# Kernel tuning notes

Hardware: AMD Instinct MI355X
Metric: run time of the kernel (lower is better)

The kernel has to match this reference:

```python
import jax, jax.numpy as jnp
import numpy as np

B, N, C = 2, 2048, 1024
H = 16
R = 4
MLP = 4096
LORA_SCALE = 1.0 / R  # lora_alpha=1, r=4
EPS = 1e-5


def _ln(x, g, b):
    m = jnp.mean(x, axis=-1, keepdims=True)
    v = jnp.mean(jnp.square(x - m), axis=-1, keepdims=True)
    return (x - m) * jax.lax.rsqrt(v + EPS) * g + b


def setup_inputs() -> dict:
    key = jax.random.key(0)
    ks = jax.random.split(key, 16)
    s = lambda k, shape, fan: jax.random.normal(k, shape, jnp.float32) * (1.0 / np.sqrt(fan))
    return {
        "x": jax.random.normal(ks[0], (B, N, C), jnp.float32),
        "pos": jax.random.normal(ks[1], (B, N, C), jnp.float32),
        "Wqkv": s(ks[2], (3 * C, C), C),
        "b_qkv": jnp.zeros((3 * C,), jnp.float32),
        "lora_A": s(ks[3], (2 * R, C), C),          # rows 0:R -> q, R:2R -> v
        "lora_B": s(ks[4], (2 * C, R), R) * 0.1,     # rows 0:C -> q, C:2C -> v
        "Wproj": s(ks[5], (C, C), C),
        "b_proj": jnp.zeros((C,), jnp.float32),
        "ln1_g": jnp.ones((C,), jnp.float32),
        "ln1_b": jnp.zeros((C,), jnp.float32),
        "ln2_g": jnp.ones((C,), jnp.float32),
        "ln2_b": jnp.zeros((C,), jnp.float32),
        "W1": s(ks[6], (MLP, C), C),
        "b1": jnp.zeros((MLP,), jnp.float32),
        "W2": s(ks[7], (C, MLP), MLP),
        "b2": jnp.zeros((C,), jnp.float32),
        "idx": 0,
    }


def reference(x, pos, Wqkv, b_qkv, lora_A, lora_B, Wproj, b_proj,
              ln1_g, ln1_b, ln2_g, ln2_b, W1, b1, W2, b2, idx):
    # (dropout layers are identity in eval mode)
    x = x + pos

    # --- attention block: Residual(PreNormDrop(SelfAttention)) ---
    h = _ln(x, ln1_g, ln1_b)                              # [B,N,C]
    qkv = h @ Wqkv.T + b_qkv                              # [B,N,3C]
    # LoRA MergedLinear: low-rank update on q and v thirds only
    after_A = h @ lora_A.T                                # [B,N,2R]
    dq = after_A[..., :R] @ lora_B[:C].T * LORA_SCALE     # [B,N,C]
    dv = after_A[..., R:] @ lora_B[C:].T * LORA_SCALE     # [B,N,C]
    qkv = qkv.at[..., :C].add(dq).at[..., 2 * C:].add(dv)

    Dh = C // H
    q, k, v = [t.reshape(B, N, H, Dh).transpose(0, 2, 1, 3)
               for t in jnp.split(qkv, 3, axis=-1)]       # each [B,H,N,Dh]
    scale = Dh ** -0.5
    attn = jnp.einsum('bhid,bhjd->bhij', q, k) * scale    # [B,H,N,N]
    attn = jax.nn.softmax(attn, axis=-1)
    o = jnp.einsum('bhij,bhjd->bhid', attn, v)            # [B,H,N,Dh]
    o = o.transpose(0, 2, 1, 3).reshape(B, N, C)
    o = o @ Wproj.T + b_proj
    x = x + o

    # --- FFN block: Residual(PreNorm(FeedForward)) ---
    h2 = _ln(x, ln2_g, ln2_b)
    h2 = jax.nn.gelu(h2 @ W1.T + b1, approximate=False)
    h2 = h2 @ W2.T + b2
    return x + h2
```

## Files before the change

### kernel.cpp

```cpp
#include <hip/hip_runtime.h>
#include <hip/hip_bf16.h>
#include <math.h>

typedef __hip_bfloat16 bf16;
typedef __attribute__((ext_vector_type(4))) float f32x4;
typedef __attribute__((ext_vector_type(16))) float f32x16;
typedef __attribute__((ext_vector_type(8))) short s16x8;

__device__ __forceinline__ void async_cp16(void* lds, const void* g) {
    __builtin_amdgcn_global_load_lds((const __attribute__((address_space(1))) void*)g,
                                     (__attribute__((address_space(3))) void*)lds, 16, 0, 0);
}

__device__ __forceinline__ float gelu_fast(float x) {
    float y = 1.5957691216f * (x + 0.044715f * x * x * x);
    float t = __expf(y);
    float th = 1.0f - 2.0f / (t + 1.0f);
    return 0.5f * x * (1.0f + th);
}

__global__ __launch_bounds__(256)
void cvt_all(const float* __restrict__ w0, const float* __restrict__ w1,
             const float* __restrict__ w2, const float* __restrict__ w3,
             bf16* __restrict__ o0, bf16* __restrict__ o1,
             bf16* __restrict__ o2, bf16* __restrict__ o3) {
    int i = blockIdx.x * 256 + threadIdx.x;
    const float* src; bf16* dst; int j = i;
    if (j < 786432)            { src = w0; dst = o0; }
    else if (j < 1048576)      { j -= 786432;  src = w1; dst = o1; }
    else if (j < 2097152)      { j -= 1048576; src = w2; dst = o2; }
    else                       { j -= 2097152; src = w3; dst = o3; }
    float4 v = ((const float4*)src)[j];
    union { bf16 o[4]; uint2 u; } pk;
    pk.o[0] = __float2bfloat16(v.x); pk.o[1] = __float2bfloat16(v.y);
    pk.o[2] = __float2bfloat16(v.z); pk.o[3] = __float2bfloat16(v.w);
    ((uint2*)dst)[j] = pk.u;
}

template <bool ADD>
__global__ __launch_bounds__(256)
void ln_kernel(const float* __restrict__ xin, const float* __restrict__ pos,
               const float* __restrict__ gam, const float* __restrict__ bet,
               float* __restrict__ x1, bf16* __restrict__ hout) {
    const int row = blockIdx.x, tid = threadIdx.x;
    const size_t off = (size_t)row * 1024;
    float4 v = ((const float4*)(xin + off))[tid];
    if constexpr (ADD) {
        float4 p = ((const float4*)(pos + off))[tid];
        v.x += p.x; v.y += p.y; v.z += p.z; v.w += p.w;
        ((float4*)(x1 + off))[tid] = v;
    }
    float s  = v.x + v.y + v.z + v.w;
    float s2 = v.x*v.x + v.y*v.y + v.z*v.z + v.w*v.w;
#pragma unroll
    for (int o = 32; o >= 1; o >>= 1) { s += __shfl_xor(s, o); s2 += __shfl_xor(s2, o); }
    __shared__ float sS[4], sS2[4];
    int w = tid >> 6, lane = tid & 63;
    if (lane == 0) { sS[w] = s; sS2[w] = s2; }
    __syncthreads();
    float mean = (sS[0] + sS[1] + sS[2] + sS[3]) * (1.f / 1024.f);
    float e2   = (sS2[0] + sS2[1] + sS2[2] + sS2[3]) * (1.f / 1024.f);
    float rstd = rsqrtf(e2 - mean * mean + 1e-5f);
    float4 gv = ((const float4*)gam)[tid], bv = ((const float4*)bet)[tid];
    bf16* ho = hout + off + tid * 4;
    ho[0] = __float2bfloat16((v.x - mean) * rstd * gv.x + bv.x);
    ho[1] = __float2bfloat16((v.y - mean) * rstd * gv.y + bv.y);
    ho[2] = __float2bfloat16((v.z - mean) * rstd * gv.z + bv.z);
    ho[3] = __float2bfloat16((v.w - mean) * rstd * gv.w + bv.w);
}

template <int MODE>
__global__ __launch_bounds__(256)
void gemm_bk64(const bf16* __restrict__ A, const bf16* __restrict__ B,
               const float* __restrict__ bias, bf16* __restrict__ outp,
               int M, int N, int K) {
    __shared__ bf16 As[128 * 64];
    __shared__ bf16 Bs[128 * 64];
    const int tid = threadIdx.x;
    const int lane = tid & 63, w = tid >> 6;
    const int grp = lane >> 4, c16 = lane & 15;
    const int wm = (w & 1) * 64, wn = (w >> 1) * 64;
    const int bm = blockIdx.y * 128, bn = blockIdx.x * 128;

    f32x4 acc[4][4];
    const f32x4 zero = {0.f, 0.f, 0.f, 0.f};
#pragma unroll
    for (int mi = 0; mi < 4; mi++)
#pragma unroll
        for (int ni = 0; ni < 4; ni++) acc[mi][ni] = zero;

    for (int k0 = 0; k0 < K; k0 += 64) {
#pragma unroll
        for (int t = 0; t < 4; t++) {
            int s = t * 256 + tid;
            int row = s >> 3, db = s & 7;
            int gb = (db ^ (row & 7)) << 3;
            async_cp16(&As[s * 8], A + (size_t)(bm + row) * K + k0 + gb);
            async_cp16(&Bs[s * 8], B + (size_t)(bn + row) * K + k0 + gb);
        }
        __syncthreads();
#pragma unroll
        for (int kc = 0; kc < 2; kc++) {
            s16x8 af[4], bf[4];
#pragma unroll
            for (int mi = 0; mi < 4; mi++) {
                int r = wm + mi * 16 + c16;
                af[mi] = *(const s16x8*)&As[r * 64 + ((((kc << 2) | grp) ^ (r & 7)) << 3)];
            }
#pragma unroll
            for (int ni = 0; ni < 4; ni++) {
                int r = wn + ni * 16 + c16;
                bf[ni] = *(const s16x8*)&Bs[r * 64 + ((((kc << 2) | grp) ^ (r & 7)) << 3)];
            }
#pragma unroll
            for (int mi = 0; mi < 4; mi++)
#pragma unroll
                for (int ni = 0; ni < 4; ni++)
                    acc[mi][ni] = __builtin_amdgcn_mfma_f32_16x16x32_bf16(af[mi], bf[ni], acc[mi][ni], 0, 0, 0);
        }
        __syncthreads();
    }

#pragma unroll
    for (int mi = 0; mi < 4; mi++)
#pragma unroll
        for (int ni = 0; ni < 4; ni++) {
            int r0 = bm + wm + mi * 16 + grp * 4;
            int c  = bn + wn + ni * 16 + c16;
            float bv = bias[c];
#pragma unroll
            for (int q = 0; q < 4; q++) {
                size_t idx = (size_t)(r0 + q) * N + c;
                float v = acc[mi][ni][q] + bv;
                if constexpr (MODE == 2) v = gelu_fast(v);
                outp[idx] = __float2bfloat16(v);
            }
        }
}

__global__ __launch_bounds__(256)
void gemm_n64(const bf16* __restrict__ A, const bf16* __restrict__ B,
              const float* __restrict__ bias, const float* __restrict__ resid,
              float* __restrict__ outp, int M, int N, int K) {
    __shared__ bf16 As[128 * 64];
    __shared__ bf16 Bs[64 * 64];
    const int tid = threadIdx.x;
    const int lane = tid & 63, w = tid >> 6;
    const int grp = lane >> 4, c16 = lane & 15;
    const int wm = w * 32;
    const int bm = blockIdx.y * 128, bn = blockIdx.x * 64;

    f32x4 acc[2][4];
    const f32x4 zero = {0.f, 0.f, 0.f, 0.f};
#pragma unroll
    for (int mi = 0; mi < 2; mi++)
#pragma unroll
        for (int ni = 0; ni < 4; ni++) acc[mi][ni] = zero;

    for (int k0 = 0; k0 < K; k0 += 64) {
#pragma unroll
        for (int t = 0; t < 4; t++) {
            int s = t * 256 + tid;
            int row = s >> 3, db = s & 7;
            async_cp16(&As[s * 8], A + (size_t)(bm + row) * K + k0 + ((db ^ (row & 7)) << 3));
        }
#pragma unroll
        for (int t = 0; t < 2; t++) {
            int s = t * 256 + tid;
            int row = s >> 3, db = s & 7;
            async_cp16(&Bs[s * 8], B + (size_t)(bn + row) * K + k0 + ((db ^ (row & 7)) << 3));
        }
        __syncthreads();
#pragma unroll
        for (int kc = 0; kc < 2; kc++) {
            s16x8 af[2], bf[4];
#pragma unroll
            for (int mi = 0; mi < 2; mi++) {
                int r = wm + mi * 16 + c16;
                af[mi] = *(const s16x8*)&As[r * 64 + ((((kc << 2) | grp) ^ (r & 7)) << 3)];
            }
#pragma unroll
            for (int ni = 0; ni < 4; ni++) {
                int rb = ni * 16 + c16;
                bf[ni] = *(const s16x8*)&Bs[rb * 64 + ((((kc << 2) | grp) ^ (rb & 7)) << 3)];
            }
#pragma unroll
            for (int mi = 0; mi < 2; mi++)
#pragma unroll
                for (int ni = 0; ni < 4; ni++)
                    acc[mi][ni] = __builtin_amdgcn_mfma_f32_16x16x32_bf16(af[mi], bf[ni], acc[mi][ni], 0, 0, 0);
        }
        __syncthreads();
    }

#pragma unroll
    for (int mi = 0; mi < 2; mi++)
#pragma unroll
        for (int ni = 0; ni < 4; ni++) {
            int r0 = bm + wm + mi * 16 + grp * 4;
            int c  = bn + ni * 16 + c16;
            float bv = bias[c];
#pragma unroll
            for (int q = 0; q < 4; q++) {
                size_t idx = (size_t)(r0 + q) * N + c;
                outp[idx] = acc[mi][ni][q] + bv + resid[idx];
            }
        }
}

__global__ __launch_bounds__(256)
void lora_a_kernel(const bf16* __restrict__ h, const float* __restrict__ A,
                   float* __restrict__ afterA) {
    const int row = blockIdx.x, tid = threadIdx.x;
    float hv[4];
#pragma unroll
    for (int t = 0; t < 4; t++) hv[t] = __bfloat162float(h[(size_t)row * 1024 + tid * 4 + t]);
    float p[8];
#pragma unroll
    for (int r = 0; r < 8; r++) {
        float4 av = ((const float4*)(A + (size_t)r * 1024))[tid];
        p[r] = hv[0] * av.x + hv[1] * av.y + hv[2] * av.z + hv[3] * av.w;
    }
#pragma unroll
    for (int r = 0; r < 8; r++)
#pragma unroll
        for (int o = 32; o >= 1; o >>= 1) p[r] += __shfl_xor(p[r], o);
    __shared__ float red[4][8];
    int w = tid >> 6, lane = tid & 63;
    if (lane == 0) {
#pragma unroll
        for (int r = 0; r < 8; r++) red[w][r] = p[r];
    }
    __syncthreads();
    if (tid < 8) afterA[(size_t)row * 8 + tid] = red[0][tid] + red[1][tid] + red[2][tid] + red[3][tid];
}

__global__ __launch_bounds__(256)
void attn_prep(const bf16* __restrict__ qkv, const float* __restrict__ afterA,
               const float* __restrict__ loraB, bf16* __restrict__ Qb,
               bf16* __restrict__ Kb, bf16* __restrict__ Vt) {
    const int bh = blockIdx.y, b = bh >> 4, h = bh & 15;
    const int it = blockIdx.x;
    __shared__ bf16 Vs[64 * 65];
    const int tid = threadIdx.x;
#pragma unroll
    for (int t = 0; t < 16; t++) {
        int s = t * 256 + tid;
        int il = s >> 6, d = s & 63;
        int ig = b * 2048 + it * 64 + il;
        size_t grow = (size_t)ig * 3072 + h * 64 + d;
        int col = h * 64 + d;
        const float* aA = afterA + (size_t)ig * 8;
        float4 bq = ((const float4*)loraB)[col];
        float4 bvv = ((const float4*)loraB)[1024 + col];
        float dq = (aA[0]*bq.x  + aA[1]*bq.y  + aA[2]*bq.z  + aA[3]*bq.w)  * 0.25f;
        float dv = (aA[4]*bvv.x + aA[5]*bvv.y + aA[6]*bvv.z + aA[7]*bvv.w) * 0.25f;
        float q = (__bfloat162float(qkv[grow]) + dq) * 0.18033688011f;
        float k = __bfloat162float(qkv[grow + 1024]);
        float v = __bfloat162float(qkv[grow + 2048]) + dv;
        size_t orow = (size_t)(bh * 2048 + it * 64 + il) * 64 + d;
        Qb[orow] = __float2bfloat16(q);
        Kb[orow] = __float2bfloat16(k);
        Vs[d * 65 + il] = __float2bfloat16(v);
    }
    __syncthreads();
#pragma unroll
    for (int t = 0; t < 16; t++) {
        int s = t * 256 + tid;
        int d = s >> 6, il = s & 63;
        Vt[(size_t)(bh * 64 + d) * 2048 + it * 64 + il] = Vs[d * 65 + il];
    }
}

__global__ __launch_bounds__(256)
void attn_fused(const bf16* __restrict__ Qb, const bf16* __restrict__ Kb,
                const bf16* __restrict__ Vt, bf16* __restrict__ Og) {
    __shared__ bf16 Qs[128 * 64], Ks[64 * 64], Vs[64 * 64];
    const int tid = threadIdx.x;
    const int lane = tid & 63, w = tid >> 6;
    const int c32 = lane & 31, l5 = lane >> 5;
    const int bh = blockIdx.y, b = bh >> 4, h = bh & 15;
    const int i0 = blockIdx.x * 128;
    const int rowperm = (c32 & 19) | (((c32 >> 3) & 1) << 2) | (((c32 >> 2) & 1) << 3);

    const size_t qbase = (size_t)(bh * 2048 + i0) * 64;
#pragma unroll
    for (int t = 0; t < 4; t++) {
        int s = t * 256 + tid;
        int row = s >> 3, db = s & 7;
        async_cp16(&Qs[s * 8], Qb + qbase + row * 64 + ((db ^ (row & 7)) << 3));
    }
    __syncthreads();
    s16x8 qf[4];
    {
        int rq = w * 32 + c32;
#pragma unroll
        for (int kc = 0; kc < 4; kc++) {
            int db = 2 * kc + l5;
            qf[kc] = *(const s16x8*)&Qs[rq * 64 + ((db ^ (rq & 7)) << 3)];
        }
    }

    f32x16 Oq[2];
#pragma unroll
    for (int dq = 0; dq < 2; dq++)
#pragma unroll
        for (int r = 0; r < 16; r++) Oq[dq][r] = 0.f;
    float l_lane = 0.f;

    for (int j0 = 0; j0 < 2048; j0 += 64) {
        __syncthreads();
#pragma unroll
        for (int t = 0; t < 2; t++) {
            int s = t * 256 + tid;
            int row = s >> 3, db = s & 7;
            int gb = (db ^ (row & 7)) << 3;
            async_cp16(&Ks[s * 8], Kb + (size_t)(bh * 2048 + j0 + row) * 64 + gb);
            async_cp16(&Vs[s * 8], Vt + (size_t)(bh * 64 + row) * 2048 + j0 + gb);
        }
        __syncthreads();

        f32x16 Sq[2];
#pragma unroll
        for (int jq = 0; jq < 2; jq++) {
#pragma unroll
            for (int r = 0; r < 16; r++) Sq[jq][r] = 0.f;
            int rk = jq * 32 + rowperm;
#pragma unroll
            for (int kc = 0; kc < 4; kc++) {
                int db = 2 * kc + l5;
                s16x8 af = *(const s16x8*)&Ks[rk * 64 + ((db ^ (rk & 7)) << 3)];
                Sq[jq] = __builtin_amdgcn_mfma_f32_32x32x16_bf16(af, qf[kc], Sq[jq], 0, 0, 0);
            }
        }

        s16x8 pf[4];
#pragma unroll
        for (int kc = 0; kc < 4; kc++) {
            union { s16x8 v; bf16 e[8]; } u;
#pragma unroll
            for (int jj = 0; jj < 8; jj++) {
                float p = exp2f(Sq[kc >> 1][8 * (kc & 1) + jj]);
                l_lane += p;
                u.e[jj] = __float2bfloat16(p);
            }
            pf[kc] = u.v;
        }

#pragma unroll
        for (int dq = 0; dq < 2; dq++) {
            int rd = dq * 32 + c32;
#pragma unroll
            for (int kc = 0; kc < 4; kc++) {
                int jb = 2 * kc + l5;
                s16x8 af = *(const s16x8*)&Vs[rd * 64 + ((jb ^ (rd & 7)) << 3)];
                Oq[dq] = __builtin_amdgcn_mfma_f32_32x32x16_bf16(af, pf[kc], Oq[dq], 0, 0, 0);
            }
        }
    }

    float l = l_lane + __shfl_xor(l_lane, 32);
    float inv = 1.0f / fmaxf(l, 1e-35f);
    int i = i0 + w * 32 + c32;
    size_t obase = (size_t)(b * 2048 + i) * 1024 + h * 64;
#pragma unroll
    for (int dq = 0; dq < 2; dq++)
#pragma unroll
        for (int rg = 0; rg < 4; rg++) {
            union { bf16 e[4]; uint2 u; } pk;
#pragma unroll
            for (int c = 0; c < 4; c++)
                pk.e[c] = __float2bfloat16(Oq[dq][rg * 4 + c] * inv);
            int d0 = dq * 32 + l5 * 4 + rg * 8;
            *(uint2*)&Og[obase + d0] = pk.u;
        }
}

extern "C" void kernel_launch(void* const* d_in, const int* in_sizes, int n_in,
                              void* d_out, int out_size, void* d_ws, size_t ws_size,
                              hipStream_t stream) {
    const float* x     = (const float*)d_in[0];
    const float* pos   = (const float*)d_in[1];
    const float* Wqkv  = (const float*)d_in[2];
    const float* bqkv  = (const float*)d_in[3];
    const float* loraA = (const float*)d_in[4];
    const float* loraB = (const float*)d_in[5];
    const float* Wproj = (const float*)d_in[6];
    const float* bproj = (const float*)d_in[7];
    const float* ln1g  = (const float*)d_in[8];
    const float* ln1b  = (const float*)d_in[9];
    const float* ln2g  = (const float*)d_in[10];
    const float* ln2b  = (const float*)d_in[11];
    const float* W1    = (const float*)d_in[12];
    const float* b1    = (const float*)d_in[13];
    const float* W2    = (const float*)d_in[14];
    const float* b2    = (const float*)d_in[15];

    char* ws = (char*)d_ws;
    float* x1     = (float*)(ws + 0);
    bf16*  hbuf   = (bf16*) (ws + 16777216);
    bf16*  qkv    = (bf16*) (ws + 25165824);
    bf16*  gbuf   = (bf16*) (ws + 50331648);
    float* afterA = (float*)(ws + 83886080);
    bf16*  Qb     = (bf16*) (ws + 84017152);
    bf16*  Kb     = (bf16*) (ws + 92405760);
    bf16*  Vt     = (bf16*) (ws + 100794368);
    bf16*  Obf    = (bf16*) (ws + 109182976);
    bf16*  Wqkvb  = (bf16*) (ws + 117571584);
    bf16*  Wprojb = (bf16*) (ws + 123863040);
    bf16*  W1b    = (bf16*) (ws + 125960192);
    bf16*  W2b    = (bf16*) (ws + 134348800);

    cvt_all<<<12288, 256, 0, stream>>>(Wqkv, Wproj, W1, W2, Wqkvb, Wprojb, W1b, W2b);

    ln_kernel<true><<<4096, 256, 0, stream>>>(x, pos, ln1g, ln1b, x1, hbuf);

    gemm_bk64<0><<<dim3(24, 32), 256, 0, stream>>>(hbuf, Wqkvb, bqkv, qkv, 4096, 3072, 1024);

    lora_a_kernel<<<4096, 256, 0, stream>>>(hbuf, loraA, afterA);

    attn_prep<<<dim3(32, 32), 256, 0, stream>>>(qkv, afterA, loraB, Qb, Kb, Vt);
    attn_fused<<<dim3(16, 32), 256, 0, stream>>>(Qb, Kb, Vt, Obf);

    gemm_n64<<<dim3(16, 32), 256, 0, stream>>>(Obf, Wprojb, bproj, x1, x1, 4096, 1024, 1024);

    ln_kernel<false><<<4096, 256, 0, stream>>>(x1, nullptr, ln2g, ln2b, nullptr, hbuf);

    gemm_bk64<2><<<dim3(32, 32), 256, 0, stream>>>(hbuf, W1b, b1, gbuf, 4096, 4096, 1024);

    gemm_n64<<<dim3(16, 32), 256, 0, stream>>>(gbuf, W2b, b2, x1, (float*)d_out, 4096, 1024, 4096);

    (void)in_sizes; (void)n_in; (void)out_size; (void)ws_size;
}
```

Measured before the change: 409.6 us.

## Double-buffer LDS in GEMM kernels and remap workgroups across XCDs

Both GEMM kernels now use two LDS buffers and issue the async global-to-LDS loads for the next K tile before computing on the current one. This hides load latency behind MFMA work and leaves one barrier per iteration instead of two. Workgroup IDs are also remapped with a modulo-8 swizzle so that neighbouring tiles, which share A and B data, land on the same XCD for better L2 reuse. The cost is double the LDS per block, which may reduce occupancy, particularly for gemm_bk64 at 64KB.

```diff
diff --git a/kernel.cpp b/kernel.cpp
--- a/kernel.cpp
+++ b/kernel.cpp
@@ -73,14 +73,16 @@
 __global__ __launch_bounds__(256)
 void gemm_bk64(const bf16* __restrict__ A, const bf16* __restrict__ B,
                const float* __restrict__ bias, bf16* __restrict__ outp,
-               int M, int N, int K) {
-    __shared__ bf16 As[128 * 64];
-    __shared__ bf16 Bs[128 * 64];
+               int M, int N, int K, int gx) {
+    __shared__ bf16 As[2][128 * 64];
+    __shared__ bf16 Bs[2][128 * 64];
     const int tid = threadIdx.x;
     const int lane = tid & 63, w = tid >> 6;
     const int grp = lane >> 4, c16 = lane & 15;
     const int wm = (w & 1) * 64, wn = (w >> 1) * 64;
-    const int bm = blockIdx.y * 128, bn = blockIdx.x * 128;
+    const int nwg = gridDim.x, bid = blockIdx.x;
+    const int sw = (bid & 7) * (nwg >> 3) + (bid >> 3);
+    const int bm = (sw / gx) * 128, bn = (sw % gx) * 128;
 
     f32x4 acc[4][4];
     const f32x4 zero = {0.f, 0.f, 0.f, 0.f};
@@ -89,37 +91,52 @@
 #pragma unroll
         for (int ni = 0; ni < 4; ni++) acc[mi][ni] = zero;
 
-    for (int k0 = 0; k0 < K; k0 += 64) {
-#pragma unroll
-        for (int t = 0; t < 4; t++) {
-            int s = t * 256 + tid;
-            int row = s >> 3, db = s & 7;
-            int gb = (db ^ (row & 7)) << 3;
-            async_cp16(&As[s * 8], A + (size_t)(bm + row) * K + k0 + gb);
-            async_cp16(&Bs[s * 8], B + (size_t)(bn + row) * K + k0 + gb);
-        }
+#define STAGE128(bufi, k0)                                                          \
+    {                                                                               \
+        const int buf_ = (bufi);                                                    \
+        const int koff_ = (k0);                                                     \
+        _Pragma("unroll") for (int t_ = 0; t_ < 4; t_++) {                          \
+            int s_ = t_ * 256 + tid;                                                \
+            int row_ = s_ >> 3, db_ = s_ & 7;                                       \
+            int gb_ = (db_ ^ (row_ & 7)) << 3;                                      \
+            async_cp16(&As[buf_][s_ * 8], A + (size_t)(bm + row_) * K + koff_ + gb_); \
+            async_cp16(&Bs[buf_][s_ * 8], B + (size_t)(bn + row_) * K + koff_ + gb_); \
+        }                                                                           \
+    }
+
+#define COMPUTE128(bufi)                                                            \
+    {                                                                               \
+        const int buf_ = (bufi);                                                    \
+        _Pragma("unroll") for (int kc_ = 0; kc_ < 2; kc_++) {                       \
+            s16x8 af_[4], bfv_[4];                                                  \
+            _Pragma("unroll") for (int mi_ = 0; mi_ < 4; mi_++) {                   \
+                int r_ = wm + mi_ * 16 + c16;                                       \
+                af_[mi_] = *(const s16x8*)&As[buf_][r_ * 64 + ((((kc_ << 2) | grp) ^ (r_ & 7)) << 3)]; \
+            }                                                                       \
+            _Pragma("unroll") for (int ni_ = 0; ni_ < 4; ni_++) {                   \
+                int r_ = wn + ni_ * 16 + c16;                                       \
+                bfv_[ni_] = *(const s16x8*)&Bs[buf_][r_ * 64 + ((((kc_ << 2) | grp) ^ (r_ & 7)) << 3)]; \
+            }                                                                       \
+            _Pragma("unroll") for (int mi_ = 0; mi_ < 4; mi_++)                     \
+                _Pragma("unroll") for (int ni_ = 0; ni_ < 4; ni_++)                 \
+                    acc[mi_][ni_] = __builtin_amdgcn_mfma_f32_16x16x32_bf16(af_[mi_], bfv_[ni_], acc[mi_][ni_], 0, 0, 0); \
+        }                                                                           \
+    }
+
+    STAGE128(0, 0);
+    __syncthreads();
+    const int nk = K >> 6;
+    int cur = 0;
+    for (int t = 0; t < nk - 1; t++) {
+        STAGE128(cur ^ 1, (t + 1) << 6);
+        COMPUTE128(cur);
         __syncthreads();
-#pragma unroll
-        for (int kc = 0; kc < 2; kc++) {
-            s16x8 af[4], bf[4];
-#pragma unroll
-            for (int mi = 0; mi < 4; mi++) {
-                int r = wm + mi * 16 + c16;
-                af[mi] = *(const s16x8*)&As[r * 64 + ((((kc << 2) | grp) ^ (r & 7)) << 3)];
-            }
-#pragma unroll
-            for (int ni = 0; ni < 4; ni++) {
-                int r = wn + ni * 16 + c16;
-                bf[ni] = *(const s16x8*)&Bs[r * 64 + ((((kc << 2) | grp) ^ (r & 7)) << 3)];
-            }
-#pragma unroll
-            for (int mi = 0; mi < 4; mi++)
-#pragma unroll
-                for (int ni = 0; ni < 4; ni++)
-                    acc[mi][ni] = __builtin_amdgcn_mfma_f32_16x16x32_bf16(af[mi], bf[ni], acc[mi][ni], 0, 0, 0);
-        }
-        __syncthreads();
-    }
+        cur ^= 1;
+    }
+    COMPUTE128(cur);
+
+#undef STAGE128
+#undef COMPUTE128
 
 #pragma unroll
     for (int mi = 0; mi < 4; mi++)
@@ -141,14 +158,16 @@
 __global__ __launch_bounds__(256)
 void gemm_n64(const bf16* __restrict__ A, const bf16* __restrict__ B,
               const float* __restrict__ bias, const float* __restrict__ resid,
-              float* __restrict__ outp, int M, int N, int K) {
-    __shared__ bf16 As[128 * 64];
-    __shared__ bf16 Bs[64 * 64];
+              float* __restrict__ outp, int M, int N, int K, int gx) {
+    __shared__ bf16 As[2][128 * 64];
+    __shared__ bf16 Bs[2][64 * 64];
     const int tid = threadIdx.x;
     const int lane = tid & 63, w = tid >> 6;
     const int grp = lane >> 4, c16 = lane & 15;
     const int wm = w * 32;
-    const int bm = blockIdx.y * 128, bn = blockIdx.x * 64;
+    const int nwg = gridDim.x, bid = blockIdx.x;
+    const int sw = (bid & 7) * (nwg >> 3) + (bid >> 3);
+    const int bm = (sw / gx) * 128, bn = (sw % gx) * 64;
 
     f32x4 acc[2][4];
     const f32x4 zero = {0.f, 0.f, 0.f, 0.f};
@@ -157,41 +176,55 @@
 #pragma unroll
         for (int ni = 0; ni < 4; ni++) acc[mi][ni] = zero;
 
-    for (int k0 = 0; k0 < K; k0 += 64) {
-#pragma unroll
-        for (int t = 0; t < 4; t++) {
-            int s = t * 256 + tid;
-            int row = s >> 3, db = s & 7;
-            async_cp16(&As[s * 8], A + (size_t)(bm + row) * K + k0 + ((db ^ (row & 7)) << 3));
-        }
-#pragma unroll
-        for (int t = 0; t < 2; t++) {
-            int s = t * 256 + tid;
-            int row = s >> 3, db = s & 7;
-            async_cp16(&Bs[s * 8], B + (size_t)(bn + row) * K + k0 + ((db ^ (row & 7)) << 3));
-        }
+#define STAGE64(bufi, k0)                                                           \
+    {                                                                               \
+        const int buf_ = (bufi);                                                    \
+        const int koff_ = (k0);                                                     \
+        _Pragma("unroll") for (int t_ = 0; t_ < 4; t_++) {                          \
+            int s_ = t_ * 256 + tid;                                                \
+            int row_ = s_ >> 3, db_ = s_ & 7;                                       \
+            async_cp16(&As[buf_][s_ * 8], A + (size_t)(bm + row_) * K + koff_ + ((db_ ^ (row_ & 7)) << 3)); \
+        }                                                                           \
+        _Pragma("unroll") for (int t_ = 0; t_ < 2; t_++) {                          \
+            int s_ = t_ * 256 + tid;                                                \
+            int row_ = s_ >> 3, db_ = s_ & 7;                                       \
+            async_cp16(&Bs[buf_][s_ * 8], B + (size_t)(bn + row_) * K + koff_ + ((db_ ^ (row_ & 7)) << 3)); \
+        }                                                                           \
+    }
+
+#define COMPUTE64(bufi)                                                             \
+    {                                                                               \
+        const int buf_ = (bufi);                                                    \
+        _Pragma("unroll") for (int kc_ = 0; kc_ < 2; kc_++) {                       \
+            s16x8 af_[2], bfv_[4];                                                  \
+            _Pragma("unroll") for (int mi_ = 0; mi_ < 2; mi_++) {                   \
+                int r_ = wm + mi_ * 16 + c16;                                       \
+                af_[mi_] = *(const s16x8*)&As[buf_][r_ * 64 + ((((kc_ << 2) | grp) ^ (r_ & 7)) << 3)]; \
+            }                                                                       \
+            _Pragma("unroll") for (int ni_ = 0; ni_ < 4; ni_++) {                   \
+                int rb_ = ni_ * 16 + c16;                                           \
+                bfv_[ni_] = *(const s16x8*)&Bs[buf_][rb_ * 64 + ((((kc_ << 2) | grp) ^ (rb_ & 7)) << 3)]; \
+            }                                                                       \
+            _Pragma("unroll") for (int mi_ = 0; mi_ < 2; mi_++)                     \
+                _Pragma("unroll") for (int ni_ = 0; ni_ < 4; ni_++)                 \
+                    acc[mi_][ni_] = __builtin_amdgcn_mfma_f32_16x16x32_bf16(af_[mi_], bfv_[ni_], acc[mi_][ni_], 0, 0, 0); \
+        }                                                                           \
+    }
+
+    STAGE64(0, 0);
+    __syncthreads();
+    const int nk = K >> 6;
+    int cur = 0;
+    for (int t = 0; t < nk - 1; t++) {
+        STAGE64(cur ^ 1, (t + 1) << 6);
+        COMPUTE64(cur);
         __syncthreads();
-#pragma unroll
-        for (int kc = 0; kc < 2; kc++) {
-            s16x8 af[2], bf[4];
-#pragma unroll
-            for (int mi = 0; mi < 2; mi++) {
-                int r = wm + mi * 16 + c16;
-                af[mi] = *(const s16x8*)&As[r * 64 + ((((kc << 2) | grp) ^ (r & 7)) << 3)];
-            }
-#pragma unroll
-            for (int ni = 0; ni < 4; ni++) {
-                int rb = ni * 16 + c16;
-                bf[ni] = *(const s16x8*)&Bs[rb * 64 + ((((kc << 2) | grp) ^ (rb & 7)) << 3)];
-            }
-#pragma unroll
-            for (int mi = 0; mi < 2; mi++)
-#pragma unroll
-                for (int ni = 0; ni < 4; ni++)
-                    acc[mi][ni] = __builtin_amdgcn_mfma_f32_16x16x32_bf16(af[mi], bf[ni], acc[mi][ni], 0, 0, 0);
-        }
-        __syncthreads();
-    }
+        cur ^= 1;
+    }
+    COMPUTE64(cur);
+
+#undef STAGE64
+#undef COMPUTE64
 
 #pragma unroll
     for (int mi = 0; mi < 2; mi++)
@@ -415,20 +448,20 @@
 
     ln_kernel<true><<<4096, 256, 0, stream>>>(x, pos, ln1g, ln1b, x1, hbuf);
 
-    gemm_bk64<0><<<dim3(24, 32), 256, 0, stream>>>(hbuf, Wqkvb, bqkv, qkv, 4096, 3072, 1024);
+    gemm_bk64<0><<<768, 256, 0, stream>>>(hbuf, Wqkvb, bqkv, qkv, 4096, 3072, 1024, 24);
 
     lora_a_kernel<<<4096, 256, 0, stream>>>(hbuf, loraA, afterA);
 
     attn_prep<<<dim3(32, 32), 256, 0, stream>>>(qkv, afterA, loraB, Qb, Kb, Vt);
     attn_fused<<<dim3(16, 32), 256, 0, stream>>>(Qb, Kb, Vt, Obf);
 
-    gemm_n64<<<dim3(16, 32), 256, 0, stream>>>(Obf, Wprojb, bproj, x1, x1, 4096, 1024, 1024);
+    gemm_n64<<<512, 256, 0, stream>>>(Obf, Wprojb, bproj, x1, x1, 4096, 1024, 1024, 16);
 
     ln_kernel<false><<<4096, 256, 0, stream>>>(x1, nullptr, ln2g, ln2b, nullptr, hbuf);
 
-    gemm_bk64<2><<<dim3(32, 32), 256, 0, stream>>>(hbuf, W1b, b1, gbuf, 4096, 4096, 1024);
-
-    gemm_n64<<<dim3(16, 32), 256, 0, stream>>>(gbuf, W2b, b2, x1, (float*)d_out, 4096, 1024, 4096);
+    gemm_bk64<2><<<1024, 256, 0, stream>>>(hbuf, W1b, b1, gbuf, 4096, 4096, 1024, 32);
+
+    gemm_n64<<<512, 256, 0, stream>>>(gbuf, W2b, b2, x1, (float*)d_out, 4096, 1024, 4096, 16);
 
     (void)in_sizes; (void)n_in; (void)out_size; (void)ws_size;
 }
```

After: 412.6 us. No clear change (+0.7%).
